# Performance work log

Hardware: AMD Instinct MI355X
Metric: run time of the kernel (lower is better)

## Reference

```python
import jax, jax.numpy as jnp
import numpy as np
import math

NUM_HEADS = 32
NUM_KV_HEADS = 8
HEAD_DIM = 128
HIDDEN = 4096
BATCH = 2
SEQ = 2048
MASK_MIN = -1e9


def _rope(x, cos, sin):
    # x: [B, S, H, D], cos/sin: [S, D/2]
    d2 = x.shape[-1] // 2
    x1, x2 = x[..., :d2], x[..., d2:]
    c = cos[None, :, None, :]
    s = sin[None, :, None, :]
    return jnp.concatenate([x1 * c - x2 * s, x2 * c + x1 * s], axis=-1)


def setup_inputs() -> dict:
    key = jax.random.key(0)
    k1, k2, k3 = jax.random.split(key, 3)
    hidden_states = jax.random.normal(k1, (BATCH, SEQ, HIDDEN), dtype=jnp.float32) * 0.02
    Wqkv = jax.random.normal(k2, (HIDDEN, (NUM_HEADS + 2 * NUM_KV_HEADS) * HEAD_DIM), dtype=jnp.float32) * (HIDDEN ** -0.5)
    Wo = jax.random.normal(k3, (NUM_HEADS * HEAD_DIM, HIDDEN), dtype=jnp.float32) * (HIDDEN ** -0.5)
    pos = np.arange(SEQ, dtype=np.float32)
    inv_freq = 1.0 / (10000.0 ** (np.arange(0, HEAD_DIM, 2, dtype=np.float32) / HEAD_DIM))
    freqs = np.outer(pos, inv_freq)  # [S, D/2]
    cos = jnp.asarray(np.cos(freqs), dtype=jnp.float32)
    sin = jnp.asarray(np.sin(freqs), dtype=jnp.float32)
    # causal additive mask [B, 1, S, S]
    causal = np.triu(np.full((SEQ, SEQ), MASK_MIN, dtype=np.float32), k=1)
    attention_mask = jnp.broadcast_to(jnp.asarray(causal)[None, None], (BATCH, 1, SEQ, SEQ))
    return {"hidden_states": hidden_states, "Wqkv": Wqkv, "Wo": Wo,
            "cos": cos, "sin": sin, "attention_mask": attention_mask}


def reference(hidden_states, Wqkv, Wo, cos, sin, attention_mask):
    B, S, H = hidden_states.shape
    n_rep = NUM_HEADS // NUM_KV_HEADS
    qkv = jnp.einsum('bsh,hd->bsd', hidden_states, Wqkv)
    q_end = NUM_HEADS * HEAD_DIM
    k_end = q_end + NUM_KV_HEADS * HEAD_DIM
    q = qkv[..., :q_end].reshape(B, S, NUM_HEADS, HEAD_DIM)
    k = qkv[..., q_end:k_end].reshape(B, S, NUM_KV_HEADS, HEAD_DIM)
    v = qkv[..., k_end:].reshape(B, S, NUM_KV_HEADS, HEAD_DIM)
    q = _rope(q, cos, sin)
    k = _rope(k, cos, sin)
    # repeat_kv: expand kv heads to query heads
    k = jnp.repeat(k, n_rep, axis=2)  # [B, S, NH, D]
    v = jnp.repeat(v, n_rep, axis=2)
    scores = jnp.einsum('bqhd,bkhd->bhqk', q, k) / math.sqrt(HEAD_DIM)
    scores = scores + attention_mask
    scores = jnp.maximum(scores, jnp.finfo(scores.dtype).min)
    probs = jax.nn.softmax(scores.astype(jnp.float32), axis=-1).astype(q.dtype)
    attn = jnp.einsum('bhqk,bkhd->bqhd', probs, v)  # [B, S, NH, D]
    attn = attn.reshape(B, S, NUM_HEADS * HEAD_DIM)
    return jnp.einsum('bsd,dh->bsh', attn, Wo)
```

## Files before the change

### kernel.cpp

```cpp
#include <hip/hip_runtime.h>

typedef unsigned short u16;
typedef __bf16 bf16x8 __attribute__((ext_vector_type(8)));
typedef float f32x4 __attribute__((ext_vector_type(4)));
typedef float f32x16 __attribute__((ext_vector_type(16)));
typedef u16 u16x4 __attribute__((ext_vector_type(4)));

#define SEQ 2048
#define NQKV 6144
#define HID 4096

__device__ inline u16 f2bf(float f) {
  union { float f; unsigned u; } x; x.f = f;
  unsigned r = x.u + 0x7fffu + ((x.u >> 16) & 1u);
  return (u16)(r >> 16);
}
__device__ inline float bf2f(u16 u) {
  union { unsigned u; float f; } x; x.u = ((unsigned)u) << 16;
  return x.f;
}
__device__ inline f32x16 mfma32(bf16x8 a, bf16x8 b, f32x16 c) {
  return __builtin_amdgcn_mfma_f32_32x32x16_bf16(a, b, c, 0, 0, 0);
}
__device__ inline unsigned cvtpk(float lo, float hi) {
  unsigned r;
  asm("v_cvt_pk_bf16_f32 %0, %1, %2" : "=v"(r) : "v"(lo), "v"(hi));
  return r;
}
__device__ inline void gload16(const void* g, void* l) {
  __builtin_amdgcn_global_load_lds((const __attribute__((address_space(1))) void*)g,
                                   (__attribute__((address_space(3))) void*)l,
                                   16, 0, 0);
}


__global__ __launch_bounds__(256) void conv_kernel(const float* __restrict__ in,
                                                   u16* __restrict__ out) {
  int i = (blockIdx.x * 256 + threadIdx.x) * 4;
  int m = i >> 12, k = i & 4095;
  float4 v = *(const float4*)(in + i);
  u16x4 o;
  o[0] = f2bf(v.x); o[1] = f2bf(v.y); o[2] = f2bf(v.z); o[3] = f2bf(v.w);
  int p = m >> 8, r = m & 255;
  int t = k >> 5, kc = (k >> 3) & 3, e = k & 7;
  int slot = ((r >> 5) << 7) + (kc << 5) + (r & 31);
  *(u16x4*)(out + ((size_t)(p * 128 + t) * 1024 + slot) * 8 + e) = o;
}

__global__ __launch_bounds__(256) void transconv_qkv_kernel(const float* __restrict__ in,
                                                            u16* __restrict__ out) {
  __shared__ u16 tile[32][33];
  int c0 = blockIdx.x * 32, r0 = blockIdx.y * 32;
  int tx = threadIdx.x & 31, ty = threadIdx.x >> 5;
  for (int i = 0; i < 4; ++i)
    tile[ty + 8 * i][tx] = f2bf(in[(size_t)(r0 + ty + 8 * i) * NQKV + c0 + tx]);
  __syncthreads();
  int t = r0 >> 5;
  for (int i = 0; i < 4; ++i) {
    int n = c0 + ty + 8 * i;
    int p = n / 384, pc = n - p * 384;
    int kc = tx >> 3, e = tx & 7;
    int slot = ((pc >> 5) << 7) + (kc << 5) + (pc & 31);
    out[((size_t)(p * 128 + t) * 1536 + slot) * 8 + e] = tile[tx][ty + 8 * i];
  }
}

__global__ __launch_bounds__(256) void transconv_wo_kernel(const float* __restrict__ in,
                                                           u16* __restrict__ out) {
  __shared__ u16 tile[32][33];
  int c0 = blockIdx.x * 32, r0 = blockIdx.y * 32;
  int tx = threadIdx.x & 31, ty = threadIdx.x >> 5;
  for (int i = 0; i < 4; ++i)
    tile[ty + 8 * i][tx] = f2bf(in[(size_t)(r0 + ty + 8 * i) * HID + c0 + tx]);
  __syncthreads();
  int t = r0 >> 5;
  for (int i = 0; i < 4; ++i) {
    int n = c0 + ty + 8 * i;
    int p = n >> 8, pc = n & 255;
    int kc = tx >> 3, e = tx & 7;
    int slot = ((pc >> 5) << 7) + (kc << 5) + (pc & 31);
    out[((size_t)(p * 128 + t) * 1024 + slot) * 8 + e] = tile[tx][ty + 8 * i];
  }
}

__global__ __launch_bounds__(512, 2) void gemm32_kernel(const u16* __restrict__ At,
                                                        const u16* __restrict__ Btl,
                                                        u16* __restrict__ C,
                                                        int M, int N, int K, int nby) {
  __shared__ __align__(16) u16 As[3][256 * 32];
  __shared__ __align__(16) u16 Bs[3][384 * 32];
  int nwg = gridDim.x;
  int bid = blockIdx.x;
  int s = (bid & 7) * (nwg >> 3) + (bid >> 3);
  int by = s % nby, bx = s / nby;
  int row0 = by * 256, col0 = bx * 384;
  int tid = threadIdx.x, w = tid >> 6, l = tid & 63;
  int wm = w >> 2, wn = w & 3;
  int l31 = l & 31, lh = l >> 5;
  const u16* Ap = At + (size_t)by * 128 * 1024 * 8;
  const u16* Bp = Btl + (size_t)bx * 128 * 1536 * 8;
  int nkt = K >> 5;

  f32x16 acc[4][3] = {};

#define STA32(tt, bf)                                                         \
  { _Pragma("unroll")                                                         \
    for (int j = 0; j < 2; ++j) {                                             \
      int cid = j * 512 + tid;                                                \
      gload16(Ap + ((size_t)(tt) * 1024 + cid) * 8, &As[bf][cid * 8]);        \
    } }
#define STB32(tt, bf)                                                         \
  { _Pragma("unroll")                                                         \
    for (int j = 0; j < 3; ++j) {                                             \
      int cid = j * 512 + tid;                                                \
      gload16(Bp + ((size_t)(tt) * 1536 + cid) * 8, &Bs[bf][cid * 8]);        \
    } }
#define RA32(bf, im, ks, dst)                                                 \
  { int slot = ((wm * 4 + (im)) << 7) + (((ks) * 2 + lh) << 5) + l31;         \
    dst = *(const bf16x8*)&As[bf][slot * 8]; }
#define RB32(bf, in, ks, dst)                                                 \
  { int slot = ((wn * 3 + (in)) << 7) + (((ks) * 2 + lh) << 5) + l31;         \
    dst = *(const bf16x8*)&Bs[bf][slot * 8]; }

  STA32(0, 0); STB32(0, 0); STA32(1, 1); STB32(1, 1);
  asm volatile("s_waitcnt vmcnt(5)" ::: "memory");
  __builtin_amdgcn_s_barrier();

  int cur = 0;
  for (int t = 0; t < nkt; ++t) {
    int nb = cur + 2; if (nb >= 3) nb -= 3;
    bool pf = (t + 2 < nkt);
    bf16x8 a0, a1, a2, a3, b0, b1, b2;
    RA32(cur, 0, 0, a0); RA32(cur, 1, 0, a1); RA32(cur, 2, 0, a2); RA32(cur, 3, 0, a3);
    RB32(cur, 0, 0, b0); RB32(cur, 1, 0, b1); RB32(cur, 2, 0, b2);
    if (pf) STA32(t + 2, nb);
    __builtin_amdgcn_s_barrier();
    asm volatile("s_waitcnt lgkmcnt(0)" ::: "memory");
    __builtin_amdgcn_s_setprio(1);
    acc[0][0] = mfma32(a0, b0, acc[0][0]); acc[0][1] = mfma32(a0, b1, acc[0][1]);
    acc[0][2] = mfma32(a0, b2, acc[0][2]);
    acc[1][0] = mfma32(a1, b0, acc[1][0]); acc[1][1] = mfma32(a1, b1, acc[1][1]);
    acc[1][2] = mfma32(a1, b2, acc[1][2]);
    acc[2][0] = mfma32(a2, b0, acc[2][0]); acc[2][1] = mfma32(a2, b1, acc[2][1]);
    acc[2][2] = mfma32(a2, b2, acc[2][2]);
    acc[3][0] = mfma32(a3, b0, acc[3][0]); acc[3][1] = mfma32(a3, b1, acc[3][1]);
    acc[3][2] = mfma32(a3, b2, acc[3][2]);
    __builtin_amdgcn_s_setprio(0);
    __builtin_amdgcn_s_barrier();
    RA32(cur, 0, 1, a0); RA32(cur, 1, 1, a1); RA32(cur, 2, 1, a2); RA32(cur, 3, 1, a3);
    RB32(cur, 0, 1, b0); RB32(cur, 1, 1, b1); RB32(cur, 2, 1, b2);
    if (pf) STB32(t + 2, nb);
    __builtin_amdgcn_s_barrier();
    asm volatile("s_waitcnt lgkmcnt(0)" ::: "memory");
    __builtin_amdgcn_s_setprio(1);
    acc[0][0] = mfma32(a0, b0, acc[0][0]); acc[0][1] = mfma32(a0, b1, acc[0][1]);
    acc[0][2] = mfma32(a0, b2, acc[0][2]);
    acc[1][0] = mfma32(a1, b0, acc[1][0]); acc[1][1] = mfma32(a1, b1, acc[1][1]);
    acc[1][2] = mfma32(a1, b2, acc[1][2]);
    acc[2][0] = mfma32(a2, b0, acc[2][0]); acc[2][1] = mfma32(a2, b1, acc[2][1]);
    acc[2][2] = mfma32(a2, b2, acc[2][2]);
    acc[3][0] = mfma32(a3, b0, acc[3][0]); acc[3][1] = mfma32(a3, b1, acc[3][1]);
    acc[3][2] = mfma32(a3, b2, acc[3][2]);
    __builtin_amdgcn_s_setprio(0);
    if (pf)              { asm volatile("s_waitcnt vmcnt(5)" ::: "memory"); }
    else if (t + 1 < nkt){ asm volatile("s_waitcnt vmcnt(0)" ::: "memory"); }
    __builtin_amdgcn_s_barrier();
    cur = cur + 1 == 3 ? 0 : cur + 1;
  }
#undef STA32
#undef STB32
#undef RA32
#undef RB32

#pragma unroll
  for (int im = 0; im < 4; ++im)
#pragma unroll
    for (int in = 0; in < 3; ++in)
#pragma unroll
      for (int reg = 0; reg < 16; ++reg) {
        int row = row0 + wm * 128 + im * 32 + (reg & 3) + 8 * (reg >> 2) + 4 * lh;
        int col = col0 + wn * 96 + in * 32 + l31;
        C[(size_t)row * N + col] = f2bf(acc[im][in][reg]);
      }
}

__global__ __launch_bounds__(512, 2) void gemm32_o_kernel(const u16* __restrict__ At,
                                                          const u16* __restrict__ Btl,
                                                          float* __restrict__ C,
                                                          int M, int N, int K, int nby) {
  __shared__ __align__(16) u16 As[3][256 * 32];
  __shared__ __align__(16) u16 Bs[3][256 * 32];
  int nwg = gridDim.x;
  int bid = blockIdx.x;
  int s = (bid & 7) * (nwg >> 3) + (bid >> 3);
  int by = s % nby, bx = s / nby;
  int row0 = by * 256, col0 = bx * 256;
  int tid = threadIdx.x, w = tid >> 6, l = tid & 63;
  int wm = w >> 2, wn = w & 3;
  int l31 = l & 31, lh = l >> 5;
  const u16* Ap = At + (size_t)by * 128 * 1024 * 8;
  const u16* Bp = Btl + (size_t)bx * 128 * 1024 * 8;
  int nkt = K >> 5;

  f32x16 acc[4][2] = {};

#define STAO(tt, bf)                                                          \
  { _Pragma("unroll")                                                         \
    for (int j = 0; j < 2; ++j) {                                             \
      int cid = j * 512 + tid;                                                \
      gload16(Ap + ((size_t)(tt) * 1024 + cid) * 8, &As[bf][cid * 8]);        \
    } }
#define STBO(tt, bf)                                                          \
  { _Pragma("unroll")                                                         \
    for (int j = 0; j < 2; ++j) {                                             \
      int cid = j * 512 + tid;                                                \
      gload16(Bp + ((size_t)(tt) * 1024 + cid) * 8, &Bs[bf][cid * 8]);        \
    } }
#define RAO(bf, im, ks, dst)                                                  \
  { int slot = ((wm * 4 + (im)) << 7) + (((ks) * 2 + lh) << 5) + l31;         \
    dst = *(const bf16x8*)&As[bf][slot * 8]; }
#define RBO(bf, in, ks, dst)                                                  \
  { int slot = ((wn * 2 + (in)) << 7) + (((ks) * 2 + lh) << 5) + l31;         \
    dst = *(const bf16x8*)&Bs[bf][slot * 8]; }

  STAO(0, 0); STBO(0, 0); STAO(1, 1); STBO(1, 1);
  asm volatile("s_waitcnt vmcnt(4)" ::: "memory");
  __builtin_amdgcn_s_barrier();

  int cur = 0;
  for (int t = 0; t < nkt; ++t) {
    int nb = cur + 2; if (nb >= 3) nb -= 3;
    bool pf = (t + 2 < nkt);
    bf16x8 a0, a1, a2, a3, b0, b1;
    RAO(cur, 0, 0, a0); RAO(cur, 1, 0, a1); RAO(cur, 2, 0, a2); RAO(cur, 3, 0, a3);
    RBO(cur, 0, 0, b0); RBO(cur, 1, 0, b1);
    if (pf) STAO(t + 2, nb);
    __builtin_amdgcn_s_barrier();
    asm volatile("s_waitcnt lgkmcnt(0)" ::: "memory");
    __builtin_amdgcn_s_setprio(1);
    acc[0][0] = mfma32(a0, b0, acc[0][0]); acc[0][1] = mfma32(a0, b1, acc[0][1]);
    acc[1][0] = mfma32(a1, b0, acc[1][0]); acc[1][1] = mfma32(a1, b1, acc[1][1]);
    acc[2][0] = mfma32(a2, b0, acc[2][0]); acc[2][1] = mfma32(a2, b1, acc[2][1]);
    acc[3][0] = mfma32(a3, b0, acc[3][0]); acc[3][1] = mfma32(a3, b1, acc[3][1]);
    __builtin_amdgcn_s_setprio(0);
    __builtin_amdgcn_s_barrier();
    RAO(cur, 0, 1, a0); RAO(cur, 1, 1, a1); RAO(cur, 2, 1, a2); RAO(cur, 3, 1, a3);
    RBO(cur, 0, 1, b0); RBO(cur, 1, 1, b1);
    if (pf) STBO(t + 2, nb);
    __builtin_amdgcn_s_barrier();
    asm volatile("s_waitcnt lgkmcnt(0)" ::: "memory");
    __builtin_amdgcn_s_setprio(1);
    acc[0][0] = mfma32(a0, b0, acc[0][0]); acc[0][1] = mfma32(a0, b1, acc[0][1]);
    acc[1][0] = mfma32(a1, b0, acc[1][0]); acc[1][1] = mfma32(a1, b1, acc[1][1]);
    acc[2][0] = mfma32(a2, b0, acc[2][0]); acc[2][1] = mfma32(a2, b1, acc[2][1]);
    acc[3][0] = mfma32(a3, b0, acc[3][0]); acc[3][1] = mfma32(a3, b1, acc[3][1]);
    __builtin_amdgcn_s_setprio(0);
    if (pf)              { asm volatile("s_waitcnt vmcnt(4)" ::: "memory"); }
    else if (t + 1 < nkt){ asm volatile("s_waitcnt vmcnt(0)" ::: "memory"); }
    __builtin_amdgcn_s_barrier();
    cur = cur + 1 == 3 ? 0 : cur + 1;
  }
#undef STAO
#undef STBO
#undef RAO
#undef RBO

#pragma unroll
  for (int im = 0; im < 4; ++im)
#pragma unroll
    for (int in = 0; in < 2; ++in)
#pragma unroll
      for (int reg = 0; reg < 16; ++reg) {
        int row = row0 + wm * 128 + im * 32 + (reg & 3) + 8 * (reg >> 2) + 4 * lh;
        int col = col0 + wn * 64 + in * 32 + l31;
        C[(size_t)row * N + col] = acc[im][in][reg];
      }
}

__global__ __launch_bounds__(256) void rope_kernel(u16* __restrict__ qkv,
                                                   const float* __restrict__ cosb,
                                                   const float* __restrict__ sinb) {
  int idx = blockIdx.x * 256 + threadIdx.x;
  int d = idx & 63;
  int head = (idx >> 6) % 40;
  int m = idx / (64 * 40);
  int s = m & (SEQ - 1);
  int col = head < 32 ? head * 128 : 4096 + (head - 32) * 128;
  u16* p = qkv + (size_t)m * NQKV + col;
  float x1 = bf2f(p[d]), x2 = bf2f(p[d + 64]);
  float c = cosb[s * 64 + d], sn = sinb[s * 64 + d];
  p[d] = f2bf(x1 * c - x2 * sn);
  p[d + 64] = f2bf(x2 * c + x1 * sn);
}

__global__ __launch_bounds__(256) void vtrans_kernel(const u16* __restrict__ qkv,
                                                     u16* __restrict__ Vt) {
  __shared__ u16 tile[32][33];
  int bid = blockIdx.x;
  int dt = bid & 3;
  int st = (bid >> 2) & 63;
  int bk = bid >> 8;
  int b = bk >> 3, kvh = bk & 7;
  int tx = threadIdx.x & 31, ty = threadIdx.x >> 5;
  for (int i = 0; i < 4; ++i) {
    int s = st * 32 + ty + 8 * i;
    tile[ty + 8 * i][tx] = qkv[(size_t)(b * SEQ + s) * NQKV + 5120 + kvh * 128 + dt * 32 + tx];
  }
  __syncthreads();
  for (int i = 0; i < 4; ++i) {
    int d = dt * 32 + ty + 8 * i;
    Vt[((size_t)bk * 128 + d) * SEQ + st * 32 + tx] = tile[tx][ty + 8 * i];
  }
}

__global__ __launch_bounds__(256, 2) void flash_kernel(const u16* __restrict__ qkv,
                                                       const u16* __restrict__ Vt,
                                                       u16* __restrict__ attnT) {
  const float C2 = 0.12751740f;
  int bid = blockIdx.x;
  int bh = bid & 63;
  int pr = bid >> 6;
  int h = bh & 31;
  int b = bh >> 5;
  int w = threadIdx.x >> 6, l = threadIdx.x & 63;
  int hv = l >> 5;
  int q32 = l & 31;
  int kvh = h >> 2;

  __shared__ __align__(16) u16 Ks[2][64 * 128];
  __shared__ __align__(16) u16 Vs[2][128 * 64];

  const u16* kb = qkv + (size_t)(b * SEQ) * NQKV + 4096 + kvh * 128;
  const u16* vtb = Vt + (size_t)(b * 8 + kvh) * 128 * SEQ;

#define STAGEKV(TT, BF)                                                       \
  { _Pragma("unroll")                                                         \
    for (int i = 0; i < 4; ++i) {                                             \
      int ck = w * 4 + i;                                                     \
      int rk = ck * 4 + (l >> 4);                                             \
      gload16(kb + (size_t)((TT) * 64 + rk) * NQKV + (((l & 15) ^ (rk & 7)) * 8), \
              &Ks[BF][ck * 512]);                                             \
      int rv = ck * 8 + (l >> 3);                                             \
      gload16(vtb + (size_t)rv * SEQ + (TT) * 64 + (((l & 7) ^ (rv & 7)) * 8), \
              &Vs[BF][ck * 512]);                                             \
    } }

  for (int pass = 0; pass < 2; ++pass) {
    int qc = pass ? 15 - pr : pr;
    int q0 = qc * 128 + w * 32;
    int qg = q0 + q32;
    __syncthreads();

    bf16x8 qf[8];
    {
      const u16* qr = qkv + (size_t)(b * SEQ + qg) * NQKV + h * 128 + hv * 8;
#pragma unroll
      for (int d0 = 0; d0 < 8; ++d0) qf[d0] = *(const bf16x8*)(qr + d0 * 16);
    }
    f32x16 o[4] = {};
    float mreg = -1e30f, lreg = 0.f;
    int ktend = 2 * qc + 1;
    int mykt = 2 * qc + (w >> 1);

    STAGEKV(0, 0);
    for (int kt = 0; kt <= ktend; ++kt) {
      int buf = kt & 1;
      if (kt < ktend) {
        STAGEKV(kt + 1, buf ^ 1);
        asm volatile("s_waitcnt vmcnt(8)" ::: "memory");
      } else {
        asm volatile("s_waitcnt vmcnt(0)" ::: "memory");
      }
      __builtin_amdgcn_s_barrier();

      if (kt <= mykt) {
        f32x16 s0 = {}, s1 = {};
        int swzk = q32 & 7;
#pragma unroll
        for (int d0 = 0; d0 < 8; ++d0) {
          int sl = (((d0 * 2 + hv) ^ swzk) * 8);
          bf16x8 k0 = *(const bf16x8*)&Ks[buf][q32 * 128 + sl];
          bf16x8 k1 = *(const bf16x8*)&Ks[buf][(32 + q32) * 128 + sl];
          s0 = mfma32(k0, qf[d0], s0);
          s1 = mfma32(k1, qf[d0], s1);
        }
        if (kt == mykt) {
#pragma unroll
          for (int r = 0; r < 16; ++r) {
            int kloc = (r & 3) + 8 * (r >> 2) + 4 * hv;
            if (kt * 64 + kloc > qg) s0[r] = -1e30f;
            if (kt * 64 + 32 + kloc > qg) s1[r] = -1e30f;
          }
        }
        float pm = -1e30f;
#pragma unroll
        for (int r = 0; r < 16; ++r) {
          pm = fmaxf(pm, s0[r]);
          pm = fmaxf(pm, s1[r]);
        }
        pm = fmaxf(pm, __shfl_xor(pm, 32));
        if (!__all(pm - mreg <= 62.746f)) {
          float mnew = fmaxf(mreg, pm);
          float al = exp2f((mreg - mnew) * C2);
          lreg *= al;
#pragma unroll
          for (int r = 0; r < 16; ++r) {
            o[0][r] *= al; o[1][r] *= al; o[2][r] *= al; o[3][r] *= al;
          }
          mreg = mnew;
        }
        float rs = 0.f;
#pragma unroll
        for (int r = 0; r < 16; ++r) {
          s0[r] = exp2f((s0[r] - mreg) * C2); rs += s0[r];
          s1[r] = exp2f((s1[r] - mreg) * C2); rs += s1[r];
        }
        rs += __shfl_xor(rs, 32);
        lreg += rs;
        bf16x8 pa[4];
#define MKPA(KSI, SP, RB)                                                     \
        { unsigned wA = cvtpk(SP[(RB) + 0], SP[(RB) + 1]);                    \
          unsigned wB = cvtpk(SP[(RB) + 2], SP[(RB) + 3]);                    \
          unsigned wC = cvtpk(SP[(RB) + 4], SP[(RB) + 5]);                    \
          unsigned wD = cvtpk(SP[(RB) + 6], SP[(RB) + 7]);                    \
          unsigned sA = __shfl_xor(wA, 32), sB = __shfl_xor(wB, 32);          \
          unsigned sC = __shfl_xor(wC, 32), sD = __shfl_xor(wD, 32);          \
          union { unsigned u[4]; bf16x8 v; } pk;                              \
          pk.u[0] = hv ? sC : wA; pk.u[1] = hv ? sD : wB;                     \
          pk.u[2] = hv ? wC : sA; pk.u[3] = hv ? wD : sB;                     \
          pa[KSI] = pk.v; }
        MKPA(0, s0, 0) MKPA(1, s0, 8) MKPA(2, s1, 0) MKPA(3, s1, 8)
#undef MKPA
#pragma unroll
        for (int db = 0; db < 4; ++db) {
          int rv = db * 32 + q32;
          int swz = rv & 7;
#pragma unroll
          for (int ks = 0; ks < 4; ++ks) {
            bf16x8 vf = *(const bf16x8*)&Vs[buf][rv * 64 + (((ks * 2 + hv) ^ swz) * 8)];
            o[db] = mfma32(vf, pa[ks], o[db]);
          }
        }
      }
    }
    float invl = 1.0f / lreg;
    {
      int m = b * SEQ + qg;
      int p = m >> 8, r = m & 255;
      u16* op = attnT + ((size_t)(p * 128 + h * 4) * 1024 +
                         ((r >> 5) << 7) + (r & 31)) * 8 + 4 * hv;
#pragma unroll
      for (int db = 0; db < 4; ++db)
#pragma unroll
        for (int g = 0; g < 4; ++g) {
          unsigned w0 = cvtpk(o[db][g * 4 + 0] * invl, o[db][g * 4 + 1] * invl);
          unsigned w1 = cvtpk(o[db][g * 4 + 2] * invl, o[db][g * 4 + 3] * invl);
          uint2 val; val.x = w0; val.y = w1;
          *(uint2*)(op + db * 8192 + g * 256) = val;
        }
    }
  }
#undef STAGEKV
}

extern "C" void kernel_launch(void* const* d_in, const int* in_sizes, int n_in,
                              void* d_out, int out_size, void* d_ws, size_t ws_size,
                              hipStream_t stream) {
  const float* hidden = (const float*)d_in[0];
  const float* Wqkv = (const float*)d_in[1];
  const float* Wo = (const float*)d_in[2];
  const float* cosb = (const float*)d_in[3];
  const float* sinb = (const float*)d_in[4];
  float* out = (float*)d_out;

  char* ws = (char*)d_ws;
  u16* R1 = (u16*)ws;
  u16* R2 = (u16*)(ws + 50331648);
  u16* R3 = (u16*)(ws + 100663296);

  conv_kernel<<<16384, 256, 0, stream>>>(hidden, R3);
  transconv_qkv_kernel<<<dim3(6144 / 32, 4096 / 32), 256, 0, stream>>>(Wqkv, R1);
  gemm32_kernel<<<256, 512, 0, stream>>>(R3, R1, R2, 4096, 6144, 4096, 16);
  rope_kernel<<<40960, 256, 0, stream>>>(R2, cosb, sinb);
  vtrans_kernel<<<4096, 256, 0, stream>>>(R2, R3);
  flash_kernel<<<512, 256, 0, stream>>>(R2, R3, R1);
  transconv_wo_kernel<<<dim3(4096 / 32, 4096 / 32), 256, 0, stream>>>(Wo, R2);
  gemm32_o_kernel<<<256, 512, 0, stream>>>(R1, R2, out, 4096, 4096, 4096, 16);
}
```

Baseline: 522.7 us.

## Switch GEMMs to double-buffered LDS pipeline and vectorize RoPE kernel

Both GEMM kernels drop from a 3-stage LDS ring with prefetch distance 2 to a 2-stage double buffer that prefetches the next tile's A and B together, waiting on vmcnt(0) at the end of each iteration. This cuts LDS use, which could raise occupancy or ease scheduling, but it exposes more global-load latency because there is less lookahead. Separately, the RoPE kernel handles 4 elements per thread with vectorized bf16 and float4 loads, using a quarter of the blocks, to cut memory instruction count.

```diff
diff --git a/kernel.cpp b/kernel.cpp
--- a/kernel.cpp
+++ b/kernel.cpp
@@ -87,8 +87,8 @@
                                                         const u16* __restrict__ Btl,
                                                         u16* __restrict__ C,
                                                         int M, int N, int K, int nby) {
-  __shared__ __align__(16) u16 As[3][256 * 32];
-  __shared__ __align__(16) u16 Bs[3][384 * 32];
+  __shared__ __align__(16) u16 As[2][256 * 32];
+  __shared__ __align__(16) u16 Bs[2][384 * 32];
   int nwg = gridDim.x;
   int bid = blockIdx.x;
   int s = (bid & 7) * (nwg >> 3) + (bid >> 3);
@@ -122,18 +122,17 @@
   { int slot = ((wn * 3 + (in)) << 7) + (((ks) * 2 + lh) << 5) + l31;         \
     dst = *(const bf16x8*)&Bs[bf][slot * 8]; }
 
-  STA32(0, 0); STB32(0, 0); STA32(1, 1); STB32(1, 1);
-  asm volatile("s_waitcnt vmcnt(5)" ::: "memory");
+  STA32(0, 0); STB32(0, 0);
+  asm volatile("s_waitcnt vmcnt(0)" ::: "memory");
   __builtin_amdgcn_s_barrier();
 
-  int cur = 0;
   for (int t = 0; t < nkt; ++t) {
-    int nb = cur + 2; if (nb >= 3) nb -= 3;
-    bool pf = (t + 2 < nkt);
+    int cur = t & 1;
+    bool pf = (t + 1 < nkt);
     bf16x8 a0, a1, a2, a3, b0, b1, b2;
     RA32(cur, 0, 0, a0); RA32(cur, 1, 0, a1); RA32(cur, 2, 0, a2); RA32(cur, 3, 0, a3);
     RB32(cur, 0, 0, b0); RB32(cur, 1, 0, b1); RB32(cur, 2, 0, b2);
-    if (pf) STA32(t + 2, nb);
+    if (pf) { STA32(t + 1, cur ^ 1); STB32(t + 1, cur ^ 1); }
     __builtin_amdgcn_s_barrier();
     asm volatile("s_waitcnt lgkmcnt(0)" ::: "memory");
     __builtin_amdgcn_s_setprio(1);
@@ -149,7 +148,6 @@
     __builtin_amdgcn_s_barrier();
     RA32(cur, 0, 1, a0); RA32(cur, 1, 1, a1); RA32(cur, 2, 1, a2); RA32(cur, 3, 1, a3);
     RB32(cur, 0, 1, b0); RB32(cur, 1, 1, b1); RB32(cur, 2, 1, b2);
-    if (pf) STB32(t + 2, nb);
     __builtin_amdgcn_s_barrier();
     asm volatile("s_waitcnt lgkmcnt(0)" ::: "memory");
     __builtin_amdgcn_s_setprio(1);
@@ -162,10 +160,8 @@
     acc[3][0] = mfma32(a3, b0, acc[3][0]); acc[3][1] = mfma32(a3, b1, acc[3][1]);
     acc[3][2] = mfma32(a3, b2, acc[3][2]);
     __builtin_amdgcn_s_setprio(0);
-    if (pf)              { asm volatile("s_waitcnt vmcnt(5)" ::: "memory"); }
-    else if (t + 1 < nkt){ asm volatile("s_waitcnt vmcnt(0)" ::: "memory"); }
-    __builtin_amdgcn_s_barrier();
-    cur = cur + 1 == 3 ? 0 : cur + 1;
+    if (pf) { asm volatile("s_waitcnt vmcnt(0)" ::: "memory"); }
+    __builtin_amdgcn_s_barrier();
   }
 #undef STA32
 #undef STB32
@@ -188,8 +184,8 @@
                                                           const u16* __restrict__ Btl,
                                                           float* __restrict__ C,
                                                           int M, int N, int K, int nby) {
-  __shared__ __align__(16) u16 As[3][256 * 32];
-  __shared__ __align__(16) u16 Bs[3][256 * 32];
+  __shared__ __align__(16) u16 As[2][256 * 32];
+  __shared__ __align__(16) u16 Bs[2][256 * 32];
   int nwg = gridDim.x;
   int bid = blockIdx.x;
   int s = (bid & 7) * (nwg >> 3) + (bid >> 3);
@@ -223,18 +219,17 @@
   { int slot = ((wn * 2 + (in)) << 7) + (((ks) * 2 + lh) << 5) + l31;         \
     dst = *(const bf16x8*)&Bs[bf][slot * 8]; }
 
-  STAO(0, 0); STBO(0, 0); STAO(1, 1); STBO(1, 1);
-  asm volatile("s_waitcnt vmcnt(4)" ::: "memory");
+  STAO(0, 0); STBO(0, 0);
+  asm volatile("s_waitcnt vmcnt(0)" ::: "memory");
   __builtin_amdgcn_s_barrier();
 
-  int cur = 0;
   for (int t = 0; t < nkt; ++t) {
-    int nb = cur + 2; if (nb >= 3) nb -= 3;
-    bool pf = (t + 2 < nkt);
+    int cur = t & 1;
+    bool pf = (t + 1 < nkt);
     bf16x8 a0, a1, a2, a3, b0, b1;
     RAO(cur, 0, 0, a0); RAO(cur, 1, 0, a1); RAO(cur, 2, 0, a2); RAO(cur, 3, 0, a3);
     RBO(cur, 0, 0, b0); RBO(cur, 1, 0, b1);
-    if (pf) STAO(t + 2, nb);
+    if (pf) { STAO(t + 1, cur ^ 1); STBO(t + 1, cur ^ 1); }
     __builtin_amdgcn_s_barrier();
     asm volatile("s_waitcnt lgkmcnt(0)" ::: "memory");
     __builtin_amdgcn_s_setprio(1);
@@ -246,7 +241,6 @@
     __builtin_amdgcn_s_barrier();
     RAO(cur, 0, 1, a0); RAO(cur, 1, 1, a1); RAO(cur, 2, 1, a2); RAO(cur, 3, 1, a3);
     RBO(cur, 0, 1, b0); RBO(cur, 1, 1, b1);
-    if (pf) STBO(t + 2, nb);
     __builtin_amdgcn_s_barrier();
     asm volatile("s_waitcnt lgkmcnt(0)" ::: "memory");
     __builtin_amdgcn_s_setprio(1);
@@ -255,10 +249,8 @@
     acc[2][0] = mfma32(a2, b0, acc[2][0]); acc[2][1] = mfma32(a2, b1, acc[2][1]);
     acc[3][0] = mfma32(a3, b0, acc[3][0]); acc[3][1] = mfma32(a3, b1, acc[3][1]);
     __builtin_amdgcn_s_setprio(0);
-    if (pf)              { asm volatile("s_waitcnt vmcnt(4)" ::: "memory"); }
-    else if (t + 1 < nkt){ asm volatile("s_waitcnt vmcnt(0)" ::: "memory"); }
-    __builtin_amdgcn_s_barrier();
-    cur = cur + 1 == 3 ? 0 : cur + 1;
+    if (pf) { asm volatile("s_waitcnt vmcnt(0)" ::: "memory"); }
+    __builtin_amdgcn_s_barrier();
   }
 #undef STAO
 #undef STBO
@@ -281,16 +273,27 @@
                                                    const float* __restrict__ cosb,
                                                    const float* __restrict__ sinb) {
   int idx = blockIdx.x * 256 + threadIdx.x;
-  int d = idx & 63;
-  int head = (idx >> 6) % 40;
-  int m = idx / (64 * 40);
+  int d = (idx & 15) * 4;
+  int head = (idx >> 4) % 40;
+  int m = idx / (16 * 40);
   int s = m & (SEQ - 1);
   int col = head < 32 ? head * 128 : 4096 + (head - 32) * 128;
   u16* p = qkv + (size_t)m * NQKV + col;
-  float x1 = bf2f(p[d]), x2 = bf2f(p[d + 64]);
-  float c = cosb[s * 64 + d], sn = sinb[s * 64 + d];
-  p[d] = f2bf(x1 * c - x2 * sn);
-  p[d + 64] = f2bf(x2 * c + x1 * sn);
+  u16x4 x1 = *(u16x4*)(p + d);
+  u16x4 x2 = *(u16x4*)(p + d + 64);
+  float4 cv = *(const float4*)(cosb + s * 64 + d);
+  float4 sv = *(const float4*)(sinb + s * 64 + d);
+  float cc[4] = {cv.x, cv.y, cv.z, cv.w};
+  float ss[4] = {sv.x, sv.y, sv.z, sv.w};
+  u16x4 o1, o2;
+#pragma unroll
+  for (int j = 0; j < 4; ++j) {
+    float a = bf2f(x1[j]), b = bf2f(x2[j]);
+    o1[j] = f2bf(a * cc[j] - b * ss[j]);
+    o2[j] = f2bf(b * cc[j] + a * ss[j]);
+  }
+  *(u16x4*)(p + d) = o1;
+  *(u16x4*)(p + d + 64) = o2;
 }
 
 __global__ __launch_bounds__(256) void vtrans_kernel(const u16* __restrict__ qkv,
@@ -481,7 +484,7 @@
   conv_kernel<<<16384, 256, 0, stream>>>(hidden, R3);
   transconv_qkv_kernel<<<dim3(6144 / 32, 4096 / 32), 256, 0, stream>>>(Wqkv, R1);
   gemm32_kernel<<<256, 512, 0, stream>>>(R3, R1, R2, 4096, 6144, 4096, 16);
-  rope_kernel<<<40960, 256, 0, stream>>>(R2, cosb, sinb);
+  rope_kernel<<<10240, 256, 0, stream>>>(R2, cosb, sinb);
   vtrans_kernel<<<4096, 256, 0, stream>>>(R2, R3);
   flash_kernel<<<512, 256, 0, stream>>>(R2, R3, R1);
   transconv_wo_kernel<<<dim3(4096 / 32, 4096 / 32), 256, 0, stream>>>(Wo, R2);
```

Measured after the change: 519.1 us. No clear change (-0.7%).
